# Performance work log

Measured on AMD Instinct MI355X. Metric: run time of the kernel, lower is better.

## Reference

```python
import jax, jax.numpy as jnp
import numpy as np

N = 1024          # n_nodes
E = 32768         # n_edges (includes N self-loops)
EMBED = 256       # embed_dim
NHEAD = 8
NHID = EMBED // NHEAD  # 32
SLOPE = 0.2       # leaky_relu negative slope
NEG = -1e30       # mask value (finite to keep grads clean)


def setup_inputs() -> dict:
    key = jax.random.key(0)
    k1, k2, k3, k4, k5 = jax.random.split(key, 5)
    h = jax.random.normal(k1, (N, EMBED), dtype=jnp.float32)
    # self-loops first so every destination row has >=1 unmasked edge
    loops = jnp.stack([jnp.arange(N, dtype=jnp.int32)] * 2, axis=1)
    rnd = jax.random.randint(k2, (E - N, 2), 0, N, dtype=jnp.int32)
    edge_index = jnp.concatenate([loops, rnd], axis=0)  # [E, 2] = (r, c)
    W_l = jax.random.normal(k3, (EMBED, NHEAD * NHID), jnp.float32) / np.sqrt(EMBED).astype(np.float32)
    W_r = jax.random.normal(k4, (EMBED, NHEAD * NHID), jnp.float32) / np.sqrt(EMBED).astype(np.float32)
    attn_w = jax.random.normal(k5, (NHID,), jnp.float32) / np.sqrt(NHID).astype(np.float32)
    return {"h": h, "edge_index": edge_index, "W_l": W_l, "W_r": W_r, "attn_w": attn_w}


def reference(h, edge_index, W_l, W_r, attn_w):
    n = h.shape[0]
    g_l = (h @ W_l).reshape(n, NHEAD, NHID)  # [N, H, D]
    g_r = (h @ W_r).reshape(n, NHEAD, NHID)  # [N, H, D]
    # dense all-pairs GATv2 score: g_sum[i, j] = g_l[j] + g_r[i]
    # (matches g_l.repeat(n,1,1) + g_r.repeat_interleave(n, dim=0))
    g_sum = g_l[None, :, :, :] + g_r[:, None, :, :]            # [N, N, H, D]
    e = jnp.einsum('ijhd,d->ijh', jax.nn.leaky_relu(g_sum, SLOPE), attn_w)  # [N, N, H]
    # edge mask: keep only (r, c) pairs present in edge_index
    adj = jnp.zeros((n, n), dtype=bool).at[edge_index[:, 0], edge_index[:, 1]].set(True)
    e = jnp.where(adj[:, :, None], e, NEG)
    a = jax.nn.softmax(e, axis=1)                               # softmax over source nodes j
    # attention-weighted aggregation of source features, concat heads
    out = jnp.einsum('ijh,jhd->ihd', a, g_l).reshape(n, NHEAD * NHID)  # [N, EMBED]
    return out
```

## Files before the change

### kernel.cpp

```cpp
#include <hip/hip_runtime.h>
#include <hip/hip_bf16.h>
#include <stdint.h>

#define NN 1024
#define EMBED 256
#define NHEAD 8
#define NHID 32
#define SLOPE 0.2f
#define DEGMAX 64

template <int CTRL>
__device__ __forceinline__ float dpp_mov(float x) {
    int r = __builtin_amdgcn_update_dpp(0, __float_as_int(x), CTRL, 0xF, 0xF, true);
    return __int_as_float(r);
}
__device__ __forceinline__ float group32_sum(float v) {
    v += dpp_mov<0xB1>(v);
    v += dpp_mov<0x4E>(v);
    v += dpp_mov<0x141>(v);
    v += dpp_mov<0x140>(v);
    v += __shfl_xor(v, 16);
    return v;
}

__global__ __launch_bounds__(256) void k_prep(const float* __restrict__ h,
                                              const float* __restrict__ Wl,
                                              const float* __restrict__ Wr,
                                              const int* __restrict__ ei, int E,
                                              float* __restrict__ gl,
                                              float* __restrict__ gr,
                                              int* __restrict__ nbrg,
                                              int* __restrict__ cntg) {
    const int blk = blockIdx.x;
    const int t = threadIdx.x;

    if (blk < 128) {
        const int z  = blk & 1;
        const int bn = ((blk >> 1) & 3) * 64;
        const int bm = (blk >> 3) * 64;
        const float* W = z ? Wr : Wl;
        float* outg = z ? gr : gl;
        const int tx = t & 15;
        const int ty = t >> 4;

        __shared__ float As[16][68];
        __shared__ float Bs[16][68];

        float acc[4][4];
#pragma unroll
        for (int i = 0; i < 4; ++i)
#pragma unroll
            for (int j = 0; j < 4; ++j) acc[i][j] = 0.f;

        const int ar = t >> 2, ac = (t & 3) << 2;
        const int br = t >> 4, bc = (t & 15) << 2;
        const float* Ap = &h[(bm + ar) * EMBED + ac];
        const float* Bp = &W[br * EMBED + bn + bc];

        float4 a_reg = *reinterpret_cast<const float4*>(Ap);
        float4 b_reg = *reinterpret_cast<const float4*>(Bp);

        for (int k0 = 0; k0 < EMBED; k0 += 16) {
            As[ac + 0][ar] = a_reg.x; As[ac + 1][ar] = a_reg.y;
            As[ac + 2][ar] = a_reg.z; As[ac + 3][ar] = a_reg.w;
            Bs[br][bc + 0] = b_reg.x; Bs[br][bc + 1] = b_reg.y;
            Bs[br][bc + 2] = b_reg.z; Bs[br][bc + 3] = b_reg.w;
            __syncthreads();
            if (k0 + 16 < EMBED) {
                a_reg = *reinterpret_cast<const float4*>(Ap + k0 + 16);
                b_reg = *reinterpret_cast<const float4*>(Bp + (size_t)(k0 + 16) * EMBED);
            }
#pragma unroll
            for (int kk = 0; kk < 16; ++kk) {
                float4 av = *reinterpret_cast<const float4*>(&As[kk][ty * 4]);
                float4 bv = *reinterpret_cast<const float4*>(&Bs[kk][tx * 4]);
                float a[4] = {av.x, av.y, av.z, av.w};
                float b[4] = {bv.x, bv.y, bv.z, bv.w};
#pragma unroll
                for (int i = 0; i < 4; ++i)
#pragma unroll
                    for (int j = 0; j < 4; ++j) acc[i][j] += a[i] * b[j];
            }
            __syncthreads();
        }
#pragma unroll
        for (int i = 0; i < 4; ++i) {
            float4 v = make_float4(acc[i][0], acc[i][1], acc[i][2], acc[i][3]);
            *reinterpret_cast<float4*>(&outg[(bm + ty * 4 + i) * EMBED + bn + tx * 4]) = v;
        }
    } else {
        const int lo = (blk - 128) * 32;
        __shared__ unsigned int lads[1024];
#pragma unroll
        for (int u = 0; u < 4; ++u) lads[t + u * 256] = 0u;
        __syncthreads();

        const int4* ei4 = reinterpret_cast<const int4*>(ei);
        const int nvec = E >> 1;
        int base = 0;
        for (; base + 2048 <= nvec; base += 2048) {
#pragma unroll 8
            for (int u = 0; u < 8; ++u) {
                int4 v = ei4[base + u * 256 + t];
                int r0 = v.x - lo;
                if ((unsigned)r0 < 32u)
                    atomicOr(&lads[r0 * 32 + ((unsigned)v.y >> 5)], 1u << (v.y & 31));
                int r1 = v.z - lo;
                if ((unsigned)r1 < 32u)
                    atomicOr(&lads[r1 * 32 + ((unsigned)v.w >> 5)], 1u << (v.w & 31));
            }
        }
        for (int idx = base + t; idx < nvec; idx += 256) {
            int4 v = ei4[idx];
            int r0 = v.x - lo;
            if ((unsigned)r0 < 32u)
                atomicOr(&lads[r0 * 32 + ((unsigned)v.y >> 5)], 1u << (v.y & 31));
            int r1 = v.z - lo;
            if ((unsigned)r1 < 32u)
                atomicOr(&lads[r1 * 32 + ((unsigned)v.w >> 5)], 1u << (v.w & 31));
        }
        __syncthreads();

        const int wv = t >> 6, ln = t & 63;
        for (int rl = wv * 8; rl < wv * 8 + 8; ++rl) {
            unsigned int w = (ln < 32) ? lads[rl * 32 + ln] : 0u;
            int c = __popc(w);
            int pre = c;
#pragma unroll
            for (int d = 1; d < 32; d <<= 1) {
                int v = __shfl_up(pre, d);
                if (ln >= d) pre += v;
            }
            int tot = __shfl(pre, 31);
            int off = pre - c;
            if (ln == 0) cntg[lo + rl] = tot;
            while (w) {
                int b = __builtin_ctz(w);
                w &= w - 1;
                if (off < DEGMAX) nbrg[(lo + rl) * DEGMAX + off] = ln * 32 + b;
                ++off;
            }
        }
    }
}

__global__ __launch_bounds__(256) void k_attn(const float* __restrict__ gl,
                                              const float* __restrict__ gr,
                                              const int* __restrict__ nbrg,
                                              const int* __restrict__ cntg,
                                              const float* __restrict__ attn_w,
                                              float* __restrict__ out) {
    const int i = blockIdx.x;
    const int t = threadIdx.x;

    __shared__ int nbr_s[DEGMAX];
    __shared__ int cnt_sh;

    if (t == 0) cnt_sh = cntg[i];
    if (t < DEGMAX) nbr_s[t] = nbrg[i * DEGMAX + t];
    __syncthreads();

    const int cnt = cnt_sh;
    const float grv = gr[i * EMBED + t];
    const float aw = attn_w[t & 31];

    float m = -3e38f, s = 0.f, acc = 0.f;

    float g[4];
#pragma unroll
    for (int u = 0; u < 4; ++u) {
        int e = (u < cnt) ? u : cnt - 1;
        g[u] = gl[nbr_s[e] * EMBED + t];
    }

    for (int e0 = 0; e0 < cnt; e0 += 4) {
        float cg[4];
#pragma unroll
        for (int u = 0; u < 4; ++u) cg[u] = g[u];
#pragma unroll
        for (int u = 0; u < 4; ++u) {
            int e = e0 + 4 + u;
            e = (e < cnt) ? e : cnt - 1;
            g[u] = gl[nbr_s[e] * EMBED + t];
        }
        float p[4];
#pragma unroll
        for (int u = 0; u < 4; ++u) {
            float x = cg[u] + grv;
            p[u] = group32_sum((x > 0.f ? x : SLOPE * x) * aw);
        }
        float pm = p[0];
#pragma unroll
        for (int u = 1; u < 4; ++u)
            if (e0 + u < cnt) pm = fmaxf(pm, p[u]);
        float mn = fmaxf(m, pm);
        float sc = __expf(m - mn);
        float ev[4];
#pragma unroll
        for (int u = 0; u < 4; ++u)
            ev[u] = (e0 + u < cnt) ? __expf(p[u] - mn) : 0.f;
        s = s * sc + ((ev[0] + ev[1]) + (ev[2] + ev[3]));
        acc = acc * sc + ((ev[0] * cg[0] + ev[1] * cg[1]) + (ev[2] * cg[2] + ev[3] * cg[3]));
        m = mn;
    }
    out[i * EMBED + t] = acc / s;
}

extern "C" void kernel_launch(void* const* d_in, const int* in_sizes, int n_in,
                              void* d_out, int out_size, void* d_ws, size_t ws_size,
                              hipStream_t stream) {
    const float* h  = (const float*)d_in[0];
    const int*   ei = (const int*)d_in[1];
    const float* Wl = (const float*)d_in[2];
    const float* Wr = (const float*)d_in[3];
    const float* aw = (const float*)d_in[4];
    float* out = (float*)d_out;
    const int E = in_sizes[1] / 2;

    int* nbrg = (int*)d_ws;
    int* cntg = (int*)((char*)d_ws + NN * DEGMAX * 4);
    float* gl = (float*)((char*)d_ws + NN * DEGMAX * 4 + 4096);
    float* gr = gl + NN * EMBED;

    k_prep<<<160, 256, 0, stream>>>(h, Wl, Wr, ei, E, gl, gr, nbrg, cntg);
    k_attn<<<NN, 256, 0, stream>>>(gl, gr, nbrg, cntg, aw, out);
}
```

Before: 36.93 us.

## Fuse projection, adjacency build and attention into one kernel with bf16 MFMA

Replaces the two-kernel pipeline with a single kernel in which each block owns four destination rows. Each block scans the whole edge list to build its own neighbour mask. It recomputes g_l only for its gathered neighbours and g_r only for its own rows, using bf16 MFMA instead of the fp32 SIMT GEMM, then runs the online softmax from LDS. This removes a launch and the global round trip for gl, gr and the neighbour lists. In exchange every block rereads the full edge list and Wl, g_l is recomputed redundantly across blocks, and precision drops to bf16. Degree is also capped at 64, and two rows share a 128-slot neighbour tile.

```diff
diff --git a/kernel.cpp b/kernel.cpp
--- a/kernel.cpp
+++ b/kernel.cpp
@@ -4,10 +4,19 @@
 
 #define NN 1024
 #define EMBED 256
-#define NHEAD 8
-#define NHID 32
 #define SLOPE 0.2f
-#define DEGMAX 64
+
+typedef __attribute__((ext_vector_type(8))) short short8;
+typedef __attribute__((ext_vector_type(4))) float f32x4;
+
+__device__ __forceinline__ unsigned short f32_to_bf16(float f) {
+    unsigned int u = __float_as_uint(f);
+    unsigned int r = (u + 0x7FFFu + ((u >> 16) & 1u)) >> 16;
+    return (unsigned short)r;
+}
+__device__ __forceinline__ float bf16_to_f32(unsigned short h) {
+    return __uint_as_float(((unsigned int)h) << 16);
+}
 
 template <int CTRL>
 __device__ __forceinline__ float dpp_mov(float x) {
@@ -23,187 +32,237 @@
     return v;
 }
 
-__global__ __launch_bounds__(256) void k_prep(const float* __restrict__ h,
-                                              const float* __restrict__ Wl,
-                                              const float* __restrict__ Wr,
-                                              const int* __restrict__ ei, int E,
-                                              float* __restrict__ gl,
-                                              float* __restrict__ gr,
-                                              int* __restrict__ nbrg,
-                                              int* __restrict__ cntg) {
+__global__ __launch_bounds__(256, 1) void k_all(const float* __restrict__ h,
+                                                const int* __restrict__ ei, int E,
+                                                const float* __restrict__ Wl,
+                                                const float* __restrict__ Wr,
+                                                const float* __restrict__ attn_w,
+                                                float* __restrict__ out) {
     const int blk = blockIdx.x;
     const int t = threadIdx.x;
-
-    if (blk < 128) {
-        const int z  = blk & 1;
-        const int bn = ((blk >> 1) & 3) * 64;
-        const int bm = (blk >> 3) * 64;
-        const float* W = z ? Wr : Wl;
-        float* outg = z ? gr : gl;
-        const int tx = t & 15;
-        const int ty = t >> 4;
-
-        __shared__ float As[16][68];
-        __shared__ float Bs[16][68];
-
-        float acc[4][4];
-#pragma unroll
-        for (int i = 0; i < 4; ++i)
-#pragma unroll
-            for (int j = 0; j < 4; ++j) acc[i][j] = 0.f;
-
-        const int ar = t >> 2, ac = (t & 3) << 2;
-        const int br = t >> 4, bc = (t & 15) << 2;
-        const float* Ap = &h[(bm + ar) * EMBED + ac];
-        const float* Bp = &W[br * EMBED + bn + bc];
-
-        float4 a_reg = *reinterpret_cast<const float4*>(Ap);
-        float4 b_reg = *reinterpret_cast<const float4*>(Bp);
-
-        for (int k0 = 0; k0 < EMBED; k0 += 16) {
-            As[ac + 0][ar] = a_reg.x; As[ac + 1][ar] = a_reg.y;
-            As[ac + 2][ar] = a_reg.z; As[ac + 3][ar] = a_reg.w;
-            Bs[br][bc + 0] = b_reg.x; Bs[br][bc + 1] = b_reg.y;
-            Bs[br][bc + 2] = b_reg.z; Bs[br][bc + 3] = b_reg.w;
-            __syncthreads();
-            if (k0 + 16 < EMBED) {
-                a_reg = *reinterpret_cast<const float4*>(Ap + k0 + 16);
-                b_reg = *reinterpret_cast<const float4*>(Bp + (size_t)(k0 + 16) * EMBED);
-            }
-#pragma unroll
-            for (int kk = 0; kk < 16; ++kk) {
-                float4 av = *reinterpret_cast<const float4*>(&As[kk][ty * 4]);
-                float4 bv = *reinterpret_cast<const float4*>(&Bs[kk][tx * 4]);
-                float a[4] = {av.x, av.y, av.z, av.w};
-                float b[4] = {bv.x, bv.y, bv.z, bv.w};
-#pragma unroll
-                for (int i = 0; i < 4; ++i)
-#pragma unroll
-                    for (int j = 0; j < 4; ++j) acc[i][j] += a[i] * b[j];
-            }
-            __syncthreads();
-        }
-#pragma unroll
-        for (int i = 0; i < 4; ++i) {
-            float4 v = make_float4(acc[i][0], acc[i][1], acc[i][2], acc[i][3]);
-            *reinterpret_cast<float4*>(&outg[(bm + ty * 4 + i) * EMBED + bn + tx * 4]) = v;
-        }
-    } else {
-        const int lo = (blk - 128) * 32;
-        __shared__ unsigned int lads[1024];
-#pragma unroll
-        for (int u = 0; u < 4; ++u) lads[t + u * 256] = 0u;
-        __syncthreads();
-
-        const int4* ei4 = reinterpret_cast<const int4*>(ei);
+    const int rbase = blk * 4;
+    const int w = t >> 6, lane = t & 63;
+    const int l16 = lane & 15, g = lane >> 4;
+
+    __shared__ unsigned int maskL[128];
+    __shared__ int nbrL[4][64];
+    __shared__ int cntL[4];
+    __shared__ int cmap[128];
+    __shared__ __align__(16) unsigned short Ast[128 * 40];
+    __shared__ __align__(16) unsigned short Bst[256 * 40];
+    __shared__ float grL[4 * 264];
+    __shared__ unsigned short glL[128 * 272];
+
+    if (t < 128) maskL[t] = 0u;
+    __syncthreads();
+    {
+        const int4* ei4 = (const int4*)ei;
         const int nvec = E >> 1;
         int base = 0;
         for (; base + 2048 <= nvec; base += 2048) {
 #pragma unroll 8
             for (int u = 0; u < 8; ++u) {
                 int4 v = ei4[base + u * 256 + t];
-                int r0 = v.x - lo;
-                if ((unsigned)r0 < 32u)
-                    atomicOr(&lads[r0 * 32 + ((unsigned)v.y >> 5)], 1u << (v.y & 31));
-                int r1 = v.z - lo;
-                if ((unsigned)r1 < 32u)
-                    atomicOr(&lads[r1 * 32 + ((unsigned)v.w >> 5)], 1u << (v.w & 31));
+                int r0 = v.x - rbase;
+                if ((unsigned)r0 < 4u)
+                    atomicOr(&maskL[r0 * 32 + ((unsigned)v.y >> 5)], 1u << (v.y & 31));
+                int r1 = v.z - rbase;
+                if ((unsigned)r1 < 4u)
+                    atomicOr(&maskL[r1 * 32 + ((unsigned)v.w >> 5)], 1u << (v.w & 31));
             }
         }
         for (int idx = base + t; idx < nvec; idx += 256) {
             int4 v = ei4[idx];
-            int r0 = v.x - lo;
-            if ((unsigned)r0 < 32u)
-                atomicOr(&lads[r0 * 32 + ((unsigned)v.y >> 5)], 1u << (v.y & 31));
-            int r1 = v.z - lo;
-            if ((unsigned)r1 < 32u)
-                atomicOr(&lads[r1 * 32 + ((unsigned)v.w >> 5)], 1u << (v.w & 31));
-        }
+            int r0 = v.x - rbase;
+            if ((unsigned)r0 < 4u)
+                atomicOr(&maskL[r0 * 32 + ((unsigned)v.y >> 5)], 1u << (v.y & 31));
+            int r1 = v.z - rbase;
+            if ((unsigned)r1 < 4u)
+                atomicOr(&maskL[r1 * 32 + ((unsigned)v.w >> 5)], 1u << (v.w & 31));
+        }
+        if ((E & 1) && t == 0) {
+            int r = ei[2 * (E - 1)] - rbase, c = ei[2 * (E - 1) + 1];
+            if ((unsigned)r < 4u)
+                atomicOr(&maskL[r * 32 + ((unsigned)c >> 5)], 1u << (c & 31));
+        }
+    }
+    __syncthreads();
+
+    {
+        unsigned int wd = (lane < 32) ? maskL[w * 32 + lane] : 0u;
+        int c = __popc(wd);
+        int pre = c;
+#pragma unroll
+        for (int d = 1; d < 32; d <<= 1) {
+            int v = __shfl_up(pre, d);
+            if (lane >= d) pre += v;
+        }
+        int tot = __shfl(pre, 31);
+        int off = pre - c;
+        if (lane == 0) cntL[w] = tot > 64 ? 64 : tot;
+        while (wd) {
+            int b = __builtin_ctz(wd);
+            wd &= wd - 1;
+            if (off < 64) nbrL[w][off] = lane * 32 + b;
+            ++off;
+        }
+    }
+
+    {
+        f32x4 accg[4];
+#pragma unroll
+        for (int nf = 0; nf < 4; ++nf) accg[nf] = (f32x4)(0.f);
+        for (int kt = 0; kt < 8; ++kt) {
+            const int k0 = kt * 32;
+            __syncthreads();
+            if (t < 128) {
+                int m = t >> 3, q = t & 7;
+                float4 v = *(const float4*)(h + (size_t)(rbase + (m & 3)) * EMBED + k0 + 4 * q);
+                int b = m * 40 + 4 * q;
+                Ast[b + 0] = f32_to_bf16(v.x); Ast[b + 1] = f32_to_bf16(v.y);
+                Ast[b + 2] = f32_to_bf16(v.z); Ast[b + 3] = f32_to_bf16(v.w);
+            }
+            {
+                int kk = t >> 3, f = t & 7;
+                const float* src = Wr + (size_t)(k0 + kk) * EMBED;
+#pragma unroll
+                for (int j = 0; j < 8; ++j) {
+                    int n0 = (f + 8 * j) * 4;
+                    float4 v = *(const float4*)(src + n0);
+                    Bst[(n0 + 0) * 40 + kk] = f32_to_bf16(v.x);
+                    Bst[(n0 + 1) * 40 + kk] = f32_to_bf16(v.y);
+                    Bst[(n0 + 2) * 40 + kk] = f32_to_bf16(v.z);
+                    Bst[(n0 + 3) * 40 + kk] = f32_to_bf16(v.w);
+                }
+            }
+            __syncthreads();
+            short8 a = *(const short8*)&Ast[l16 * 40 + g * 8];
+#pragma unroll
+            for (int nf = 0; nf < 4; ++nf) {
+                short8 b = *(const short8*)&Bst[(64 * w + nf * 16 + l16) * 40 + g * 8];
+                accg[nf] = __builtin_amdgcn_mfma_f32_16x16x32_bf16(a, b, accg[nf], 0, 0, 0);
+            }
+        }
+        if (g == 0) {
+#pragma unroll
+            for (int nf = 0; nf < 4; ++nf)
+#pragma unroll
+                for (int p = 0; p < 4; ++p)
+                    grL[p * 264 + 64 * w + nf * 16 + l16] = accg[nf][p];
+        }
+    }
+
+    const float aw = attn_w[t & 31];
+    for (int s = 0; s < 2; ++s) {
         __syncthreads();
-
-        const int wv = t >> 6, ln = t & 63;
-        for (int rl = wv * 8; rl < wv * 8 + 8; ++rl) {
-            unsigned int w = (ln < 32) ? lads[rl * 32 + ln] : 0u;
-            int c = __popc(w);
-            int pre = c;
-#pragma unroll
-            for (int d = 1; d < 32; d <<= 1) {
-                int v = __shfl_up(pre, d);
-                if (ln >= d) pre += v;
-            }
-            int tot = __shfl(pre, 31);
-            int off = pre - c;
-            if (ln == 0) cntg[lo + rl] = tot;
-            while (w) {
-                int b = __builtin_ctz(w);
-                w &= w - 1;
-                if (off < DEGMAX) nbrg[(lo + rl) * DEGMAX + off] = ln * 32 + b;
-                ++off;
-            }
-        }
-    }
-}
-
-__global__ __launch_bounds__(256) void k_attn(const float* __restrict__ gl,
-                                              const float* __restrict__ gr,
-                                              const int* __restrict__ nbrg,
-                                              const int* __restrict__ cntg,
-                                              const float* __restrict__ attn_w,
-                                              float* __restrict__ out) {
-    const int i = blockIdx.x;
-    const int t = threadIdx.x;
-
-    __shared__ int nbr_s[DEGMAX];
-    __shared__ int cnt_sh;
-
-    if (t == 0) cnt_sh = cntg[i];
-    if (t < DEGMAX) nbr_s[t] = nbrg[i * DEGMAX + t];
-    __syncthreads();
-
-    const int cnt = cnt_sh;
-    const float grv = gr[i * EMBED + t];
-    const float aw = attn_w[t & 31];
-
-    float m = -3e38f, s = 0.f, acc = 0.f;
-
-    float g[4];
-#pragma unroll
-    for (int u = 0; u < 4; ++u) {
-        int e = (u < cnt) ? u : cnt - 1;
-        g[u] = gl[nbr_s[e] * EMBED + t];
-    }
-
-    for (int e0 = 0; e0 < cnt; e0 += 4) {
-        float cg[4];
-#pragma unroll
-        for (int u = 0; u < 4; ++u) cg[u] = g[u];
-#pragma unroll
-        for (int u = 0; u < 4; ++u) {
-            int e = e0 + 4 + u;
-            e = (e < cnt) ? e : cnt - 1;
-            g[u] = gl[nbr_s[e] * EMBED + t];
-        }
-        float p[4];
-#pragma unroll
-        for (int u = 0; u < 4; ++u) {
-            float x = cg[u] + grv;
-            p[u] = group32_sum((x > 0.f ? x : SLOPE * x) * aw);
-        }
-        float pm = p[0];
-#pragma unroll
-        for (int u = 1; u < 4; ++u)
-            if (e0 + u < cnt) pm = fmaxf(pm, p[u]);
-        float mn = fmaxf(m, pm);
-        float sc = __expf(m - mn);
-        float ev[4];
-#pragma unroll
-        for (int u = 0; u < 4; ++u)
-            ev[u] = (e0 + u < cnt) ? __expf(p[u] - mn) : 0.f;
-        s = s * sc + ((ev[0] + ev[1]) + (ev[2] + ev[3]));
-        acc = acc * sc + ((ev[0] * cg[0] + ev[1] * cg[1]) + (ev[2] * cg[2] + ev[3] * cg[3]));
-        m = mn;
-    }
-    out[i * EMBED + t] = acc / s;
+        const int c0 = cntL[2 * s], c1 = cntL[2 * s + 1];
+        if (t < 128) {
+            int v;
+            if (t < c0) v = nbrL[2 * s][t];
+            else if (t < c0 + c1) v = nbrL[2 * s + 1][t - c0];
+            else v = rbase;
+            cmap[t] = v;
+        }
+
+        f32x4 acc[8][4];
+#pragma unroll
+        for (int mt = 0; mt < 8; ++mt)
+#pragma unroll
+            for (int nf = 0; nf < 4; ++nf) acc[mt][nf] = (f32x4)(0.f);
+
+        for (int kt = 0; kt < 8; ++kt) {
+            const int k0 = kt * 32;
+            __syncthreads();
+            {
+                int m = t >> 1, j0 = (t & 1) * 16;
+                const float* src = h + (size_t)cmap[m] * EMBED + k0 + j0;
+                float4 v0 = *(const float4*)(src + 0);
+                float4 v1 = *(const float4*)(src + 4);
+                float4 v2 = *(const float4*)(src + 8);
+                float4 v3 = *(const float4*)(src + 12);
+                int b = m * 40 + j0;
+                Ast[b + 0]  = f32_to_bf16(v0.x); Ast[b + 1]  = f32_to_bf16(v0.y);
+                Ast[b + 2]  = f32_to_bf16(v0.z); Ast[b + 3]  = f32_to_bf16(v0.w);
+                Ast[b + 4]  = f32_to_bf16(v1.x); Ast[b + 5]  = f32_to_bf16(v1.y);
+                Ast[b + 6]  = f32_to_bf16(v1.z); Ast[b + 7]  = f32_to_bf16(v1.w);
+                Ast[b + 8]  = f32_to_bf16(v2.x); Ast[b + 9]  = f32_to_bf16(v2.y);
+                Ast[b + 10] = f32_to_bf16(v2.z); Ast[b + 11] = f32_to_bf16(v2.w);
+                Ast[b + 12] = f32_to_bf16(v3.x); Ast[b + 13] = f32_to_bf16(v3.y);
+                Ast[b + 14] = f32_to_bf16(v3.z); Ast[b + 15] = f32_to_bf16(v3.w);
+            }
+            {
+                int kk = t >> 3, f = t & 7;
+                const float* src = Wl + (size_t)(k0 + kk) * EMBED;
+#pragma unroll
+                for (int j = 0; j < 8; ++j) {
+                    int n0 = (f + 8 * j) * 4;
+                    float4 v = *(const float4*)(src + n0);
+                    Bst[(n0 + 0) * 40 + kk] = f32_to_bf16(v.x);
+                    Bst[(n0 + 1) * 40 + kk] = f32_to_bf16(v.y);
+                    Bst[(n0 + 2) * 40 + kk] = f32_to_bf16(v.z);
+                    Bst[(n0 + 3) * 40 + kk] = f32_to_bf16(v.w);
+                }
+            }
+            __syncthreads();
+            short8 bfr[4];
+#pragma unroll
+            for (int nf = 0; nf < 4; ++nf)
+                bfr[nf] = *(const short8*)&Bst[(64 * w + nf * 16 + l16) * 40 + g * 8];
+#pragma unroll
+            for (int mt = 0; mt < 8; ++mt) {
+                short8 a = *(const short8*)&Ast[(mt * 16 + l16) * 40 + g * 8];
+#pragma unroll
+                for (int nf = 0; nf < 4; ++nf)
+                    acc[mt][nf] = __builtin_amdgcn_mfma_f32_16x16x32_bf16(a, bfr[nf], acc[mt][nf], 0, 0, 0);
+            }
+        }
+#pragma unroll
+        for (int mt = 0; mt < 8; ++mt)
+#pragma unroll
+            for (int nf = 0; nf < 4; ++nf)
+#pragma unroll
+                for (int p = 0; p < 4; ++p)
+                    glL[(mt * 16 + g * 4 + p) * 272 + 64 * w + nf * 16 + l16] =
+                        f32_to_bf16(acc[mt][nf][p]);
+        __syncthreads();
+
+#pragma unroll
+        for (int r = 0; r < 2; ++r) {
+            const int rg = 2 * s + r;
+            const int cntr = r ? c1 : c0;
+            const int eb = r ? c0 : 0;
+            const float grv = grL[rg * 264 + t];
+            float mm = -3e38f, ss = 0.f, ac = 0.f;
+            for (int e0 = 0; e0 < cntr; e0 += 4) {
+                float cg[4], p4[4];
+#pragma unroll
+                for (int u = 0; u < 4; ++u) {
+                    int e = e0 + u;
+                    e = (e < cntr) ? e : cntr - 1;
+                    cg[u] = bf16_to_f32(glL[(eb + e) * 272 + t]);
+                }
+#pragma unroll
+                for (int u = 0; u < 4; ++u) {
+                    float x = cg[u] + grv;
+                    p4[u] = group32_sum((x > 0.f ? x : SLOPE * x) * aw);
+                }
+                float pm = p4[0];
+#pragma unroll
+                for (int u = 1; u < 4; ++u)
+                    if (e0 + u < cntr) pm = fmaxf(pm, p4[u]);
+                float mn = fmaxf(mm, pm);
+                float sc = __expf(mm - mn);
+                float ev[4];
+#pragma unroll
+                for (int u = 0; u < 4; ++u)
+                    ev[u] = (e0 + u < cntr) ? __expf(p4[u] - mn) : 0.f;
+                ss = ss * sc + ((ev[0] + ev[1]) + (ev[2] + ev[3]));
+                ac = ac * sc + ((ev[0] * cg[0] + ev[1] * cg[1]) + (ev[2] * cg[2] + ev[3] * cg[3]));
+                mm = mn;
+            }
+            out[(size_t)(rbase + rg) * EMBED + t] = ac / ss;
+        }
+    }
 }
 
 extern "C" void kernel_launch(void* const* d_in, const int* in_sizes, int n_in,
@@ -217,11 +276,5 @@
     float* out = (float*)d_out;
     const int E = in_sizes[1] / 2;
 
-    int* nbrg = (int*)d_ws;
-    int* cntg = (int*)((char*)d_ws + NN * DEGMAX * 4);
-    float* gl = (float*)((char*)d_ws + NN * DEGMAX * 4 + 4096);
-    float* gr = gl + NN * EMBED;
-
-    k_prep<<<160, 256, 0, stream>>>(h, Wl, Wr, ei, E, gl, gr, nbrg, cntg);
-    k_attn<<<NN, 256, 0, stream>>>(gl, gr, nbrg, cntg, aw, out);
-}
+    k_all<<<256, 256, 0, stream>>>(h, ei, E, Wl, Wr, aw, out);
+}
```

Measured after the change: 66.58 us. +80.3%, slower.
